# Kernel tuning notes

Hardware: AMD Instinct MI355X
Metric: run time of the kernel (lower is better)

## Reference

```python
import jax, jax.numpy as jnp
import numpy as np

MAX_LEN = 4096

def causal_mask(seq_len, dtype=jnp.float32):
    # nn.Transformer.generate_square_subsequent_mask: 0 on/below diag, -inf above
    i = jnp.arange(seq_len)[:, None]
    j = jnp.arange(seq_len)[None, :]
    return jnp.where(j > i, -jnp.inf, 0.0).astype(dtype)

def setup_inputs() -> dict:
    key = jax.random.key(0)
    kq, kk, kv = jax.random.split(key, 3)
    B, H, S, D = 2, 8, 4096, 64
    q = jax.random.normal(kq, (B, H, S, D), dtype=jnp.float32)
    k = jax.random.normal(kk, (B, H, S, D), dtype=jnp.float32)
    v = jax.random.normal(kv, (B, H, S, D), dtype=jnp.float32)
    return {"q": q, "k": k, "v": v}

def reference(q, k, v):
    # q,k,v: [B,H,S,D]. Dropout is identity in eval mode.
    S = k.shape[2]
    D = k.shape[-1]
    scale = 1.0 / jnp.sqrt(jnp.asarray(D, dtype=q.dtype))
    scores = jnp.einsum('bhqd,bhkd->bhqk', q, k) * scale  # [B,H,S,S]
    scores = scores + causal_mask(S, scores.dtype)[None, None]
    probs = jax.nn.softmax(scores, axis=-1)
    return jnp.einsum('bhqk,bhkd->bhqd', probs, v)
```

## Files before the change

### kernel.cpp

```cpp
#include <hip/hip_runtime.h>


typedef __attribute__((ext_vector_type(8)))  short short8;
typedef __attribute__((ext_vector_type(16))) float floatx16;

#define S_LEN 4096
#define D_DIM 64
#define LOG2E 1.44269504088896340736f
#define M8L2  11.541560327111385f

__device__ __forceinline__ unsigned short f2bf(float f) {
    union { float f; unsigned u; } x; x.f = f;
    unsigned u = x.u;
    u += 0x7fffu + ((u >> 16) & 1u);
    return (unsigned short)(u >> 16);
}

__device__ __forceinline__ float fast_exp2(float x) {
    float r;
    asm("v_exp_f32 %0, %1" : "=v"(r) : "v"(x));
    return r;
}

__device__ __forceinline__ void glds16(const void* g, void* l) {
    __builtin_amdgcn_global_load_lds(
        (const __attribute__((address_space(1))) unsigned int*)g,
        (__attribute__((address_space(3))) unsigned int*)l, 16, 0, 0);
}

__global__ __launch_bounds__(256) void prep_kv(
        const float* __restrict__ K, const float* __restrict__ V,
        unsigned short* __restrict__ img) {
    const int kt = blockIdx.x;
    const int bh = blockIdx.y;
    const int t  = threadIdx.x;
    const size_t inbase = (size_t)bh * (S_LEN * D_DIM) + (size_t)kt * (64 * D_DIM);
    unsigned short* out = img + ((size_t)bh * 64 + kt) * 8192;
    __shared__ __align__(16) unsigned short vt[64 * 72];
    #pragma unroll
    for (int i = 0; i < 2; ++i) {
        const int g   = i * 256 + t;
        const int key = g >> 3;
        const int d8  = (g & 7) * 8;
        const float* kp = K + inbase + key * 64 + d8;
        const float4 k0 = *(const float4*)kp;
        const float4 k1 = *(const float4*)(kp + 4);
        unsigned short ks8[8] = { f2bf(k0.x), f2bf(k0.y), f2bf(k0.z), f2bf(k0.w),
                                  f2bf(k1.x), f2bf(k1.y), f2bf(k1.z), f2bf(k1.w) };
        const int fk = (key >> 5) * 4 + (d8 >> 4);
        const int L  = ((d8 >> 3) & 1) * 32 + (key & 31);
        *(uint4*)(out + fk * 512 + L * 8) = *(const uint4*)ks8;
        const float* vp = V + inbase + key * 64 + d8;
        const float4 v0 = *(const float4*)vp;
        const float4 v1 = *(const float4*)(vp + 4);
        vt[(d8 + 0) * 72 + key] = f2bf(v0.x);
        vt[(d8 + 1) * 72 + key] = f2bf(v0.y);
        vt[(d8 + 2) * 72 + key] = f2bf(v0.z);
        vt[(d8 + 3) * 72 + key] = f2bf(v0.w);
        vt[(d8 + 4) * 72 + key] = f2bf(v1.x);
        vt[(d8 + 5) * 72 + key] = f2bf(v1.y);
        vt[(d8 + 6) * 72 + key] = f2bf(v1.z);
        vt[(d8 + 7) * 72 + key] = f2bf(v1.w);
    }
    __syncthreads();
    #pragma unroll
    for (int i = 0; i < 2; ++i) {
        const int o  = i * 256 + t;
        const int fv = o >> 6;
        const int L  = o & 63;
        const int d  = (fv >> 2) * 32 + (L & 31);
        const int kb = (fv & 3) * 16 + (L >> 5) * 8;
        *(uint4*)(out + 4096 + fv * 512 + L * 8) = *(const uint4*)&vt[d * 72 + kb];
    }
}

__global__ __launch_bounds__(256, 4) void fa_fwd(
        const float* __restrict__ Q, const unsigned short* __restrict__ img,
        float* __restrict__ O) {
    const int bh = blockIdx.x;
    const int qt = 63 - (int)blockIdx.y;
    const int tid  = threadIdx.x;
    const int wave = tid >> 6;
    const int lane = tid & 63;
    const int l31  = lane & 31;
    const int hl   = lane >> 5;
    const int wq   = wave >> 1;
    const int wk   = wave & 1;

    __shared__ __align__(16) unsigned short kv[2][8192];

    bool h1;
    {
        const unsigned pa = hl ? 0xA1u : 0xA0u;
        const unsigned pb = hl ? 0xB1u : 0xB0u;
        auto pr = __builtin_amdgcn_permlane32_swap(pa, pb, false, false);
        h1 = ((unsigned)pr[0] == (hl ? 0xA1u : 0xB1u));
    }

    const size_t base = (size_t)bh * (S_LEN * D_DIM);
    const int q0 = qt * 64;

    short8 qf[4];
    {
        const float* qp = Q + base + (size_t)(q0 + wq * 32 + l31) * D_DIM + hl * 8;
        #pragma unroll
        for (int ks = 0; ks < 4; ++ks) {
            const float4 f0 = *(const float4*)(qp + ks * 16);
            const float4 f1 = *(const float4*)(qp + ks * 16 + 4);
            short8 a;
            a[0] = (short)f2bf(f0.x * 0.125f); a[1] = (short)f2bf(f0.y * 0.125f);
            a[2] = (short)f2bf(f0.z * 0.125f); a[3] = (short)f2bf(f0.w * 0.125f);
            a[4] = (short)f2bf(f1.x * 0.125f); a[5] = (short)f2bf(f1.y * 0.125f);
            a[6] = (short)f2bf(f1.z * 0.125f); a[7] = (short)f2bf(f1.w * 0.125f);
            qf[ks] = a;
        }
    }

    floatx16 o_acc[2];
    #pragma unroll
    for (int n = 0; n < 2; ++n)
        #pragma unroll
        for (int r = 0; r < 16; ++r) o_acc[n][r] = 0.f;
    float lsum = 0.f;

    const unsigned short* tsrc = img + (size_t)bh * 64 * 8192;
    const int nkt = qt + 1;

    #define DMA_TILE(KT, BUF)                                                  \
        { const unsigned short* s_ = tsrc + (size_t)(KT) * 8192;               \
          _Pragma("unroll")                                                    \
          for (int i_ = 0; i_ < 4; ++i_) {                                     \
              const int f_ = wave * 4 + i_;                                    \
              glds16(s_ + f_ * 512 + lane * 8, (BUF) + f_ * 512 + lane * 8);   \
          } }

    DMA_TILE(0, kv[0])

    for (int kt = 0; kt < nkt; ++kt) {
        asm volatile("s_waitcnt vmcnt(0)" ::: "memory");
        __builtin_amdgcn_s_barrier();
        asm volatile("" ::: "memory");
        unsigned short* buf = kv[kt & 1];
        if (kt + 1 < nkt) DMA_TILE(kt + 1, kv[(kt + 1) & 1])

        const bool diag = (kt == nkt - 1);
        if (diag && wk > wq) continue;

        floatx16 s;
        #pragma unroll
        for (int r = 0; r < 16; ++r) s[r] = 0.f;
        #pragma unroll
        for (int ks = 0; ks < 4; ++ks) {
            const short8 ak = *(const short8*)&buf[(wk * 4 + ks) * 512 + lane * 8];
            s = __builtin_amdgcn_mfma_f32_32x32x16_bf16(ak, qf[ks], s, 0, 0, 0);
        }

        float p[16];
        #pragma unroll
        for (int r = 0; r < 16; ++r)
            p[r] = fast_exp2(fmaf(s[r], LOG2E, -M8L2));
        if (diag && wk == wq) {
            #pragma unroll
            for (int r = 0; r < 16; ++r) {
                const int row = (r & 3) + 8 * (r >> 2) + 4 * hl;
                p[r] = (row > l31) ? 0.f : p[r];
            }
        }
        #pragma unroll
        for (int r = 0; r < 16; ++r) lsum += p[r];

        unsigned w[4][2];
        #pragma unroll
        for (int rg = 0; rg < 4; ++rg) {
            w[rg][0] = __builtin_amdgcn_perm(__float_as_uint(p[rg * 4 + 1]),
                                             __float_as_uint(p[rg * 4 + 0]), 0x07060302u);
            w[rg][1] = __builtin_amdgcn_perm(__float_as_uint(p[rg * 4 + 3]),
                                             __float_as_uint(p[rg * 4 + 2]), 0x07060302u);
        }

        unsigned a0[4], a1[4];
        if (h1) {
            auto s0 = __builtin_amdgcn_permlane32_swap(w[1][0], w[0][0], false, false);
            a0[2] = (unsigned)s0[0]; a0[0] = (unsigned)s0[1];
            auto s1 = __builtin_amdgcn_permlane32_swap(w[1][1], w[0][1], false, false);
            a0[3] = (unsigned)s1[0]; a0[1] = (unsigned)s1[1];
            auto s2 = __builtin_amdgcn_permlane32_swap(w[3][0], w[2][0], false, false);
            a1[2] = (unsigned)s2[0]; a1[0] = (unsigned)s2[1];
            auto s3 = __builtin_amdgcn_permlane32_swap(w[3][1], w[2][1], false, false);
            a1[3] = (unsigned)s3[0]; a1[1] = (unsigned)s3[1];
        } else {
            auto s0 = __builtin_amdgcn_permlane32_swap(w[0][0], w[1][0], false, false);
            a0[0] = (unsigned)s0[0]; a0[2] = (unsigned)s0[1];
            auto s1 = __builtin_amdgcn_permlane32_swap(w[0][1], w[1][1], false, false);
            a0[1] = (unsigned)s1[0]; a0[3] = (unsigned)s1[1];
            auto s2 = __builtin_amdgcn_permlane32_swap(w[2][0], w[3][0], false, false);
            a1[0] = (unsigned)s2[0]; a1[2] = (unsigned)s2[1];
            auto s3 = __builtin_amdgcn_permlane32_swap(w[2][1], w[3][1], false, false);
            a1[1] = (unsigned)s3[0]; a1[3] = (unsigned)s3[1];
        }
        union Cvt { unsigned u[4]; short8 s8; };
        Cvt c0, c1;
        c0.u[0] = a0[0]; c0.u[1] = a0[1]; c0.u[2] = a0[2]; c0.u[3] = a0[3];
        c1.u[0] = a1[0]; c1.u[1] = a1[1]; c1.u[2] = a1[2]; c1.u[3] = a1[3];
        const short8 apf[2] = { c0.s8, c1.s8 };

        #pragma unroll
        for (int kk = 0; kk < 2; ++kk) {
            #pragma unroll
            for (int nt = 0; nt < 2; ++nt) {
                const short8 bv = *(const short8*)&buf[4096 + (nt * 4 + 2 * wk + kk) * 512 + lane * 8];
                o_acc[nt] = __builtin_amdgcn_mfma_f32_32x32x16_bf16(apf[kk], bv, o_acc[nt], 0, 0, 0);
            }
        }
    }
    #undef DMA_TILE

    lsum += __shfl_xor(lsum, 32);
    __syncthreads();
    float* ored = (float*)kv[0];
    float* lred = (float*)kv[1];
    if (lane < 32) lred[(wk * 2 + wq) * 32 + lane] = lsum;
    if (wk == 1) {
        #pragma unroll
        for (int nt = 0; nt < 2; ++nt)
            #pragma unroll
            for (int r = 0; r < 16; ++r) {
                const int q = (r & 3) + 8 * (r >> 2) + 4 * hl;
                ored[wq * 2048 + q * 64 + nt * 32 + l31] = o_acc[nt][r];
            }
    }
    __syncthreads();
    if (wk == 0) {
        #pragma unroll
        for (int r = 0; r < 16; ++r) {
            const int q = (r & 3) + 8 * (r >> 2) + 4 * hl;
            const float l = lred[wq * 32 + q] + lred[(2 + wq) * 32 + q];
            const float inv = 1.0f / l;
            #pragma unroll
            for (int nt = 0; nt < 2; ++nt) {
                const float v = (o_acc[nt][r] + ored[wq * 2048 + q * 64 + nt * 32 + l31]) * inv;
                O[base + (size_t)(q0 + wq * 32 + q) * D_DIM + nt * 32 + l31] = v;
            }
        }
    }
}

extern "C" void kernel_launch(void* const* d_in, const int* in_sizes, int n_in,
                              void* d_out, int out_size, void* d_ws, size_t ws_size,
                              hipStream_t stream) {
    const float* q = (const float*)d_in[0];
    const float* k = (const float*)d_in[1];
    const float* v = (const float*)d_in[2];
    float* o = (float*)d_out;
    (void)in_sizes; (void)n_in; (void)out_size; (void)ws_size;
    unsigned short* img = (unsigned short*)d_ws;
    hipLaunchKernelGGL(prep_kv, dim3(64, 16), dim3(256), 0, stream, k, v, img);
    hipLaunchKernelGGL(fa_fwd,  dim3(16, 64), dim3(256), 0, stream, q, img, o);
}
```

Before: 140.7 us.

## XOR-swizzle bf16 K/V image to cut LDS bank conflicts in attention

The prep kernel now writes the K/V fragment image with an XOR swizzle on the 16-byte lane slot, building the whole tile in shared memory and copying it out linearly. The attention kernel applies the matching inverse swizzle when reading K and V fragments from LDS. The aim is to remove LDS bank conflicts on the 128-bit fragment reads in the main loop, and to simplify the prep kernel's V transpose. Extra index arithmetic is added per load, and any mismatch between writer and reader swizzles would corrupt results.

```diff
diff --git a/kernel.cpp b/kernel.cpp
--- a/kernel.cpp
+++ b/kernel.cpp
@@ -36,41 +36,40 @@
     const int t  = threadIdx.x;
     const size_t inbase = (size_t)bh * (S_LEN * D_DIM) + (size_t)kt * (64 * D_DIM);
     unsigned short* out = img + ((size_t)bh * 64 + kt) * 8192;
-    __shared__ __align__(16) unsigned short vt[64 * 72];
+    __shared__ __align__(16) unsigned short tile[8192];
     #pragma unroll
     for (int i = 0; i < 2; ++i) {
         const int g   = i * 256 + t;
         const int key = g >> 3;
-        const int d8  = (g & 7) * 8;
+        const int a   = g & 7;
+        const int d8  = a * 8;
         const float* kp = K + inbase + key * 64 + d8;
         const float4 k0 = *(const float4*)kp;
         const float4 k1 = *(const float4*)(kp + 4);
         unsigned short ks8[8] = { f2bf(k0.x), f2bf(k0.y), f2bf(k0.z), f2bf(k0.w),
                                   f2bf(k1.x), f2bf(k1.y), f2bf(k1.z), f2bf(k1.w) };
-        const int fk = (key >> 5) * 4 + (d8 >> 4);
-        const int L  = ((d8 >> 3) & 1) * 32 + (key & 31);
-        *(uint4*)(out + fk * 512 + L * 8) = *(const uint4*)ks8;
+        const int fk = (key >> 5) * 4 + (a >> 1);
+        const int Lk = (a & 1) * 32 + (key & 31);
+        const int pk = Lk ^ ((fk & 3) << 1) ^ ((Lk >> 3) & 3);
+        *(uint4*)(tile + fk * 512 + pk * 8) = *(const uint4*)ks8;
         const float* vp = V + inbase + key * 64 + d8;
         const float4 v0 = *(const float4*)vp;
         const float4 v1 = *(const float4*)(vp + 4);
-        vt[(d8 + 0) * 72 + key] = f2bf(v0.x);
-        vt[(d8 + 1) * 72 + key] = f2bf(v0.y);
-        vt[(d8 + 2) * 72 + key] = f2bf(v0.z);
-        vt[(d8 + 3) * 72 + key] = f2bf(v0.w);
-        vt[(d8 + 4) * 72 + key] = f2bf(v1.x);
-        vt[(d8 + 5) * 72 + key] = f2bf(v1.y);
-        vt[(d8 + 6) * 72 + key] = f2bf(v1.z);
-        vt[(d8 + 7) * 72 + key] = f2bf(v1.w);
+        const float vv[8] = { v0.x, v0.y, v0.z, v0.w, v1.x, v1.y, v1.z, v1.w };
+        const int fv = 8 + (a >> 2) * 4 + (key >> 4);
+        const int jj = key & 7;
+        #pragma unroll
+        for (int j = 0; j < 8; ++j) {
+            const int Lv = ((key >> 3) & 1) * 32 + 8 * (a & 3) + j;
+            const int pv = Lv ^ ((fv & 3) << 1) ^ ((Lv >> 3) & 3);
+            tile[fv * 512 + pv * 8 + jj] = f2bf(vv[j]);
+        }
     }
     __syncthreads();
     #pragma unroll
-    for (int i = 0; i < 2; ++i) {
-        const int o  = i * 256 + t;
-        const int fv = o >> 6;
-        const int L  = o & 63;
-        const int d  = (fv >> 2) * 32 + (L & 31);
-        const int kb = (fv & 3) * 16 + (L >> 5) * 8;
-        *(uint4*)(out + 4096 + fv * 512 + L * 8) = *(const uint4*)&vt[d * 72 + kb];
+    for (int i = 0; i < 4; ++i) {
+        const int o = i * 256 + t;
+        *(uint4*)(out + o * 8) = *(const uint4*)(tile + o * 8);
     }
 }
 
@@ -86,6 +85,7 @@
     const int hl   = lane >> 5;
     const int wq   = wave >> 1;
     const int wk   = wave & 1;
+    const int laneS = lane ^ ((lane >> 3) & 3);
 
     __shared__ __align__(16) unsigned short kv[2][8192];
 
@@ -151,7 +151,7 @@
         for (int r = 0; r < 16; ++r) s[r] = 0.f;
         #pragma unroll
         for (int ks = 0; ks < 4; ++ks) {
-            const short8 ak = *(const short8*)&buf[(wk * 4 + ks) * 512 + lane * 8];
+            const short8 ak = *(const short8*)&buf[(wk * 4 + ks) * 512 + (laneS ^ (ks << 1)) * 8];
             s = __builtin_amdgcn_mfma_f32_32x32x16_bf16(ak, qf[ks], s, 0, 0, 0);
         }
 
@@ -208,7 +208,8 @@
         for (int kk = 0; kk < 2; ++kk) {
             #pragma unroll
             for (int nt = 0; nt < 2; ++nt) {
-                const short8 bv = *(const short8*)&buf[4096 + (nt * 4 + 2 * wk + kk) * 512 + lane * 8];
+                const int fv3 = 2 * wk + kk;
+                const short8 bv = *(const short8*)&buf[4096 + (nt * 4 + fv3) * 512 + (laneS ^ (fv3 << 1)) * 8];
                 o_acc[nt] = __builtin_amdgcn_mfma_f32_32x32x16_bf16(apf[kk], bv, o_acc[nt], 0, 0, 0);
             }
         }
```

New measurement: 143.1 us. No clear change (+1.7%).
